# Kernel optimization log

Measured on AMD Instinct MI355X. Metric: run time of the kernel, lower is better.

The kernel has to match this reference:

```python
import jax, jax.numpy as jnp
import numpy as np

IN_FEATURES = 4096
OUT_FEATURES = 11008
BATCH, SEQ = 8, 16


def setup_inputs() -> dict:
    key = jax.random.key(0)
    k_in, k_w, k_s, k_b = jax.random.split(key, 4)
    inp = jax.random.normal(k_in, (BATCH, SEQ, IN_FEATURES), dtype=jnp.float32)
    # int8 weights in [-128, 127], as torch.randint(-128, 127, ...)
    quantized_weights = jax.random.randint(
        k_w, (OUT_FEATURES, IN_FEATURES), -128, 127, dtype=jnp.int32
    ).astype(jnp.int8)
    scales = jax.random.normal(k_s, (OUT_FEATURES,), dtype=jnp.float32)
    bias = jax.random.normal(k_b, (1, OUT_FEATURES), dtype=jnp.float32)
    return {"input": inp, "quantized_weights": quantized_weights,
            "scales": scales, "bias": bias}


def reference(input, quantized_weights, scales, bias):
    # dequantize weight to activation dtype, then linear: y = x @ W^T
    w = quantized_weights.astype(input.dtype)  # [O, I]
    out = jnp.einsum("bsi,oi->bso", input, w)  # [B, S, O]
    out = out * scales  # per-output-channel scale
    out = out + bias    # bias shape [1, O] broadcasts
    return out
```

## Files before the change

### kernel.cpp

```cpp
#include <hip/hip_runtime.h>
#include <stdint.h>


#define M_ROWS 128
#define K_DIM  4096
#define N_DIM  11008
#define CHUNKS 64
#define NT128  (N_DIM / 128)
#define KSPLIT 8
#define CPB    (CHUNKS / KSPLIT)
#define XP_BYTES (M_ROWS * K_DIM * 2)
#define PART_U32 ((size_t)64 * N_DIM)

typedef __attribute__((ext_vector_type(8))) short bf16x8;
typedef __attribute__((ext_vector_type(4))) float f32x4;
typedef const unsigned __attribute__((address_space(1)))* gas1_t;
typedef unsigned __attribute__((address_space(3)))* las3_t;

__device__ __forceinline__ unsigned bf16_rn(float f) {
  unsigned u = __float_as_uint(f);
  return (u + 0x7FFFu + ((u >> 16) & 1u)) >> 16;
}
__device__ __forceinline__ unsigned pk2(int a, int b) {
  unsigned lo = __float_as_uint((float)a), hi = __float_as_uint((float)b);
#if __has_builtin(__builtin_amdgcn_perm)
  return __builtin_amdgcn_perm(hi, lo, 0x07060302u);
#else
  return (hi & 0xFFFF0000u) | (lo >> 16);
#endif
}

__device__ __forceinline__ void gload_lds16(const void* g, void* lds) {
#if __has_builtin(__builtin_amdgcn_global_load_lds)
  __builtin_amdgcn_global_load_lds((gas1_t)g, (las3_t)(size_t)(unsigned)(size_t)lds,
                                   16, 0, 0);
#else
  *(uint4*)lds = *(const uint4*)g;
#endif
}

#define BAR()    asm volatile("s_barrier" ::: "memory")
#define WBAR12() asm volatile("s_waitcnt vmcnt(12)\n\ts_barrier" ::: "memory")
#define WBAR6()  asm volatile("s_waitcnt vmcnt(6)\n\ts_barrier" ::: "memory")
#define WBAR0()  asm volatile("s_waitcnt vmcnt(0)\n\ts_barrier" ::: "memory")

__global__ __launch_bounds__(256) void pack_x_kernel(
    const float* __restrict__ x, unsigned short* __restrict__ xp) {
  int tid  = blockIdx.x * 256 + threadIdx.x;
  int lane = tid & 63;
  int h    = (tid >> 6) & 1;
  int mf   = (tid >> 7) & 7;
  int kk   = tid >> 10;
  int m     = mf * 16 + (lane & 15);
  int kbase = kk * 64 + h * 32 + ((lane >> 4) * 8);
  const float* src = x + (size_t)m * K_DIM + kbase;
  float4 f0 = *(const float4*)(src);
  float4 f1 = *(const float4*)(src + 4);
  float v[8] = {f0.x, f0.y, f0.z, f0.w, f1.x, f1.y, f1.z, f1.w};
  unsigned po[4];
#pragma unroll
  for (int i = 0; i < 4; ++i)
    po[i] = bf16_rn(v[2 * i]) | (bf16_rn(v[2 * i + 1]) << 16);
  *(uint4*)(xp + (size_t)tid * 8) = *(uint4*)po;
}

struct BReg { uint4 v[4]; };

__global__ __launch_bounds__(512, 4) void gemm8w_kernel(
    const unsigned short* __restrict__ xp,
    const int* __restrict__ wq,
    unsigned* __restrict__ part) {
  __shared__ char As[3 * 16384];

  const int tid  = threadIdx.x;
  const int lane = tid & 63;
  const int w    = tid >> 6;
  const int nt   = blockIdx.x;
  const int kz   = blockIdx.y;
  const int kk0  = kz * CPB;
  const size_t n0 = (size_t)nt * 128 + (size_t)w * 16;
  const int l15 = lane & 15, lh = lane >> 4;

  const char* agp = (const char*)xp + (size_t)kk0 * 16384 + tid * 16;
  const int* bptr = wq + (n0 + (size_t)l15) * K_DIM + (size_t)kk0 * 64 + lh * 8;

  f32x4 acc[8];
  {
    f32x4 z = {0.f, 0.f, 0.f, 0.f};
#pragma unroll
    for (int i = 0; i < 8; ++i) acc[i] = z;
  }

  auto STAGE = [&](int t, int bufOff) {
    gload_lds16(agp + (size_t)t * 16384,        As + bufOff + tid * 16);
    gload_lds16(agp + (size_t)t * 16384 + 8192, As + bufOff + tid * 16 + 8192);
  };
  auto LOADB = [&](int t, BReg& R) {
    const int* bp = bptr + t * 64;
    R.v[0] = *(const uint4*)(bp);
    R.v[1] = *(const uint4*)(bp + 4);
    R.v[2] = *(const uint4*)(bp + 32);
    R.v[3] = *(const uint4*)(bp + 36);
  };
  auto COMP = [&](const char* ab, BReg& R) {
    bf16x8 cv[2];
#pragma unroll
    for (int s = 0; s < 2; ++s) {
      union { unsigned u[4]; bf16x8 b; } c;
      c.u[0] = pk2((int)R.v[s * 2].x,     (int)R.v[s * 2].y);
      c.u[1] = pk2((int)R.v[s * 2].z,     (int)R.v[s * 2].w);
      c.u[2] = pk2((int)R.v[s * 2 + 1].x, (int)R.v[s * 2 + 1].y);
      c.u[3] = pk2((int)R.v[s * 2 + 1].z, (int)R.v[s * 2 + 1].w);
      cv[s] = c.b;
    }
#pragma unroll
    for (int mf = 0; mf < 8; ++mf)
#pragma unroll
      for (int s = 0; s < 2; ++s) {
        bf16x8 a = *(const bf16x8*)(ab + (mf * 2 + s) * 1024 + lane * 16);
        acc[mf] = __builtin_amdgcn_mfma_f32_16x16x32_bf16(a, cv[s], acc[mf], 0, 0, 0);
      }
  };

#define PHASE(T, CBUF, NBUF, RC, RN)              \
    LOADB((T) + 2, RN);                           \
    BAR();                                        \
    STAGE((T) + 2, (NBUF) * 16384);               \
    WBAR12();                                     \
    COMP(As + (CBUF) * 16384, RC);

  BReg R0, R1, R2;
  STAGE(0, 0);
  LOADB(0, R0);
  STAGE(1, 16384);
  LOADB(1, R1);

#pragma unroll 1
  for (int t = 0; t < 6; t += 3) {
    PHASE(t + 0, 0, 2, R0, R2);
    PHASE(t + 1, 1, 0, R1, R0);
    PHASE(t + 2, 2, 1, R2, R1);
  }
  WBAR6();
  COMP(As + 0 * 16384, R0);
  WBAR0();
  COMP(As + 1 * 16384, R1);
#undef PHASE

  unsigned* pb = part + (size_t)kz * PART_U32 + n0 + l15;
#pragma unroll
  for (int mf = 0; mf < 8; ++mf) {
    const int mb = mf * 16 + lh * 4;
    unsigned u0 = bf16_rn(acc[mf][0]) | (bf16_rn(acc[mf][1]) << 16);
    unsigned u1 = bf16_rn(acc[mf][2]) | (bf16_rn(acc[mf][3]) << 16);
    pb[(size_t)(mb >> 1) * N_DIM]       = u0;
    pb[(size_t)((mb >> 1) + 1) * N_DIM] = u1;
  }
}

__global__ __launch_bounds__(256) void reduce_kernel(
    const unsigned* __restrict__ part, const float* __restrict__ scales,
    const float* __restrict__ bias, float* __restrict__ out) {
  const int mp = blockIdx.y;
  const int c4 = blockIdx.x * 256 + threadIdx.x;
  if (c4 >= N_DIM / 4) return;
  const size_t n = (size_t)c4 * 4;
  float s0[4] = {0.f, 0.f, 0.f, 0.f};
  float s1[4] = {0.f, 0.f, 0.f, 0.f};
#pragma unroll
  for (int z = 0; z < KSPLIT; ++z) {
    uint4 q = *(const uint4*)(part + (size_t)z * PART_U32 + (size_t)mp * N_DIM + n);
    const unsigned uu[4] = {q.x, q.y, q.z, q.w};
#pragma unroll
    for (int j = 0; j < 4; ++j) {
      s0[j] += __uint_as_float(uu[j] << 16);
      s1[j] += __uint_as_float(uu[j] & 0xFFFF0000u);
    }
  }
  float4 sc = *(const float4*)(scales + n);
  float4 bi = *(const float4*)(bias + n);
  const float scv[4] = {sc.x, sc.y, sc.z, sc.w};
  const float biv[4] = {bi.x, bi.y, bi.z, bi.w};
  float4 r0, r1;
  float* o0 = out + (size_t)(2 * mp) * N_DIM + n;
  float* o1 = out + (size_t)(2 * mp + 1) * N_DIM + n;
  r0.x = scv[0] * s0[0] + biv[0];  r1.x = scv[0] * s1[0] + biv[0];
  r0.y = scv[1] * s0[1] + biv[1];  r1.y = scv[1] * s1[1] + biv[1];
  r0.z = scv[2] * s0[2] + biv[2];  r1.z = scv[2] * s1[2] + biv[2];
  r0.w = scv[3] * s0[3] + biv[3];  r1.w = scv[3] * s1[3] + biv[3];
  *(float4*)o0 = r0;
  *(float4*)o1 = r1;
}

__global__ __launch_bounds__(256) void naive_kernel(
    const float* __restrict__ x, const int* __restrict__ wq,
    const float* __restrict__ scales, const float* __restrict__ bias,
    float* __restrict__ out) {
  const int n = blockIdx.x * 256 + threadIdx.x;
  const int m = blockIdx.y;
  const float* xr = x + (size_t)m * K_DIM;
  const int* wr = wq + (size_t)n * K_DIM;
  float s = 0.f;
  for (int k = 0; k < K_DIM; k += 4) {
    float4 xv = *(const float4*)(xr + k);
    int4  wv = *(const int4*)(wr + k);
    s += xv.x * (float)wv.x + xv.y * (float)wv.y +
         xv.z * (float)wv.z + xv.w * (float)wv.w;
  }
  out[(size_t)m * N_DIM + n] = scales[n] * s + bias[n];
}

extern "C" void kernel_launch(void* const* d_in, const int* in_sizes, int n_in,
                              void* d_out, int out_size, void* d_ws, size_t ws_size,
                              hipStream_t stream) {
  const float* x      = (const float*)d_in[0];
  const int* wq       = (const int*)d_in[1];
  const float* scales = (const float*)d_in[2];
  const float* bias   = (const float*)d_in[3];
  float* out          = (float*)d_out;

  const size_t need = (size_t)XP_BYTES + (size_t)KSPLIT * PART_U32 * 4;
  if (ws_size < need) {
    naive_kernel<<<dim3(N_DIM / 256, M_ROWS), 256, 0, stream>>>(x, wq, scales, bias, out);
    return;
  }
  unsigned short* xp = (unsigned short*)d_ws;
  unsigned* part     = (unsigned*)((char*)d_ws + XP_BYTES);

  pack_x_kernel<<<256, 256, 0, stream>>>(x, xp);
  gemm8w_kernel<<<dim3(NT128, KSPLIT), 512, 0, stream>>>(xp, wq, part);
  reduce_kernel<<<dim3((N_DIM / 4 + 255) / 256, 64), 256, 0, stream>>>(
      part, scales, bias, out);
}
```

Baseline: 51.54 us.

## Convert GEMM to persistent blocks pulling work items from an atomic counter

The GEMM launch changes from one block per (N-tile, K-split) pair, 86x8 = 688 blocks, to 512 persistent blocks. Each block takes work items dynamically through a global atomic counter, which the pack kernel resets to zero. The aim is to spread the tail of the 688 items more evenly and reduce launch and wave-quantization imbalance. In exchange it adds an atomic and two block barriers per item, and items are ordered N-tile first so concurrent blocks share K-slices of x.

```diff
diff --git a/kernel.cpp b/kernel.cpp
--- a/kernel.cpp
+++ b/kernel.cpp
@@ -9,7 +9,11 @@
 #define NT128  (N_DIM / 128)
 #define KSPLIT 8
 #define CPB    (CHUNKS / KSPLIT)
+#define NITEMS (NT128 * KSPLIT)
+#define GBLOCKS 512
 #define XP_BYTES (M_ROWS * K_DIM * 2)
+#define CTR_OFF  XP_BYTES
+#define PART_OFF (XP_BYTES + 256)
 #define PART_U32 ((size_t)64 * N_DIM)
 
 typedef __attribute__((ext_vector_type(8))) short bf16x8;
@@ -45,7 +49,9 @@
 #define WBAR0()  asm volatile("s_waitcnt vmcnt(0)\n\ts_barrier" ::: "memory")
 
 __global__ __launch_bounds__(256) void pack_x_kernel(
-    const float* __restrict__ x, unsigned short* __restrict__ xp) {
+    const float* __restrict__ x, unsigned short* __restrict__ xp,
+    int* __restrict__ counter) {
+  if (blockIdx.x == 0 && threadIdx.x == 0) *counter = 0;
   int tid  = blockIdx.x * 256 + threadIdx.x;
   int lane = tid & 63;
   int h    = (tid >> 6) & 1;
@@ -69,58 +75,68 @@
 __global__ __launch_bounds__(512, 4) void gemm8w_kernel(
     const unsigned short* __restrict__ xp,
     const int* __restrict__ wq,
-    unsigned* __restrict__ part) {
+    unsigned* __restrict__ part,
+    int* __restrict__ counter) {
   __shared__ char As[3 * 16384];
+  __shared__ int itemLds;
 
   const int tid  = threadIdx.x;
   const int lane = tid & 63;
   const int w    = tid >> 6;
-  const int nt   = blockIdx.x;
-  const int kz   = blockIdx.y;
-  const int kk0  = kz * CPB;
-  const size_t n0 = (size_t)nt * 128 + (size_t)w * 16;
   const int l15 = lane & 15, lh = lane >> 4;
 
-  const char* agp = (const char*)xp + (size_t)kk0 * 16384 + tid * 16;
-  const int* bptr = wq + (n0 + (size_t)l15) * K_DIM + (size_t)kk0 * 64 + lh * 8;
-
-  f32x4 acc[8];
-  {
-    f32x4 z = {0.f, 0.f, 0.f, 0.f};
-#pragma unroll
-    for (int i = 0; i < 8; ++i) acc[i] = z;
-  }
-
-  auto STAGE = [&](int t, int bufOff) {
-    gload_lds16(agp + (size_t)t * 16384,        As + bufOff + tid * 16);
-    gload_lds16(agp + (size_t)t * 16384 + 8192, As + bufOff + tid * 16 + 8192);
-  };
-  auto LOADB = [&](int t, BReg& R) {
-    const int* bp = bptr + t * 64;
-    R.v[0] = *(const uint4*)(bp);
-    R.v[1] = *(const uint4*)(bp + 4);
-    R.v[2] = *(const uint4*)(bp + 32);
-    R.v[3] = *(const uint4*)(bp + 36);
-  };
-  auto COMP = [&](const char* ab, BReg& R) {
-    bf16x8 cv[2];
-#pragma unroll
-    for (int s = 0; s < 2; ++s) {
-      union { unsigned u[4]; bf16x8 b; } c;
-      c.u[0] = pk2((int)R.v[s * 2].x,     (int)R.v[s * 2].y);
-      c.u[1] = pk2((int)R.v[s * 2].z,     (int)R.v[s * 2].w);
-      c.u[2] = pk2((int)R.v[s * 2 + 1].x, (int)R.v[s * 2 + 1].y);
-      c.u[3] = pk2((int)R.v[s * 2 + 1].z, (int)R.v[s * 2 + 1].w);
-      cv[s] = c.b;
-    }
-#pragma unroll
-    for (int mf = 0; mf < 8; ++mf)
+  for (;;) {
+    if (tid == 0) itemLds = atomicAdd(counter, 1);
+    __syncthreads();
+    const int item = itemLds;
+    __syncthreads();
+    if (item >= NITEMS) return;
+
+    const int nt = item % NT128;
+    const int kz = item / NT128;
+    const int kk0 = kz * CPB;
+    const size_t n0 = (size_t)nt * 128 + (size_t)w * 16;
+
+    const char* agp = (const char*)xp + (size_t)kk0 * 16384 + tid * 16;
+    const int* bptr = wq + (n0 + (size_t)l15) * K_DIM + (size_t)kk0 * 64 + lh * 8;
+
+    f32x4 acc[8];
+    {
+      f32x4 z = {0.f, 0.f, 0.f, 0.f};
+#pragma unroll
+      for (int i = 0; i < 8; ++i) acc[i] = z;
+    }
+
+    auto STAGE = [&](int t, int bufOff) {
+      gload_lds16(agp + (size_t)t * 16384,        As + bufOff + tid * 16);
+      gload_lds16(agp + (size_t)t * 16384 + 8192, As + bufOff + tid * 16 + 8192);
+    };
+    auto LOADB = [&](int t, BReg& R) {
+      const int* bp = bptr + t * 64;
+      R.v[0] = *(const uint4*)(bp);
+      R.v[1] = *(const uint4*)(bp + 4);
+      R.v[2] = *(const uint4*)(bp + 32);
+      R.v[3] = *(const uint4*)(bp + 36);
+    };
+    auto COMP = [&](const char* ab, BReg& R) {
+      bf16x8 cv[2];
 #pragma unroll
       for (int s = 0; s < 2; ++s) {
-        bf16x8 a = *(const bf16x8*)(ab + (mf * 2 + s) * 1024 + lane * 16);
-        acc[mf] = __builtin_amdgcn_mfma_f32_16x16x32_bf16(a, cv[s], acc[mf], 0, 0, 0);
+        union { unsigned u[4]; bf16x8 b; } c;
+        c.u[0] = pk2((int)R.v[s * 2].x,     (int)R.v[s * 2].y);
+        c.u[1] = pk2((int)R.v[s * 2].z,     (int)R.v[s * 2].w);
+        c.u[2] = pk2((int)R.v[s * 2 + 1].x, (int)R.v[s * 2 + 1].y);
+        c.u[3] = pk2((int)R.v[s * 2 + 1].z, (int)R.v[s * 2 + 1].w);
+        cv[s] = c.b;
       }
-  };
+#pragma unroll
+      for (int mf = 0; mf < 8; ++mf)
+#pragma unroll
+        for (int s = 0; s < 2; ++s) {
+          bf16x8 a = *(const bf16x8*)(ab + (mf * 2 + s) * 1024 + lane * 16);
+          acc[mf] = __builtin_amdgcn_mfma_f32_16x16x32_bf16(a, cv[s], acc[mf], 0, 0, 0);
+        }
+    };
 
 #define PHASE(T, CBUF, NBUF, RC, RN)              \
     LOADB((T) + 2, RN);                           \
@@ -129,32 +145,33 @@
     WBAR12();                                     \
     COMP(As + (CBUF) * 16384, RC);
 
-  BReg R0, R1, R2;
-  STAGE(0, 0);
-  LOADB(0, R0);
-  STAGE(1, 16384);
-  LOADB(1, R1);
+    BReg R0, R1, R2;
+    STAGE(0, 0);
+    LOADB(0, R0);
+    STAGE(1, 16384);
+    LOADB(1, R1);
 
 #pragma unroll 1
-  for (int t = 0; t < 6; t += 3) {
-    PHASE(t + 0, 0, 2, R0, R2);
-    PHASE(t + 1, 1, 0, R1, R0);
-    PHASE(t + 2, 2, 1, R2, R1);
-  }
-  WBAR6();
-  COMP(As + 0 * 16384, R0);
-  WBAR0();
-  COMP(As + 1 * 16384, R1);
+    for (int t = 0; t < 6; t += 3) {
+      PHASE(t + 0, 0, 2, R0, R2);
+      PHASE(t + 1, 1, 0, R1, R0);
+      PHASE(t + 2, 2, 1, R2, R1);
+    }
+    WBAR6();
+    COMP(As + 0 * 16384, R0);
+    WBAR0();
+    COMP(As + 1 * 16384, R1);
 #undef PHASE
 
-  unsigned* pb = part + (size_t)kz * PART_U32 + n0 + l15;
-#pragma unroll
-  for (int mf = 0; mf < 8; ++mf) {
-    const int mb = mf * 16 + lh * 4;
-    unsigned u0 = bf16_rn(acc[mf][0]) | (bf16_rn(acc[mf][1]) << 16);
-    unsigned u1 = bf16_rn(acc[mf][2]) | (bf16_rn(acc[mf][3]) << 16);
-    pb[(size_t)(mb >> 1) * N_DIM]       = u0;
-    pb[(size_t)((mb >> 1) + 1) * N_DIM] = u1;
+    unsigned* pb = part + (size_t)kz * PART_U32 + n0 + l15;
+#pragma unroll
+    for (int mf = 0; mf < 8; ++mf) {
+      const int mb = mf * 16 + lh * 4;
+      unsigned u0 = bf16_rn(acc[mf][0]) | (bf16_rn(acc[mf][1]) << 16);
+      unsigned u1 = bf16_rn(acc[mf][2]) | (bf16_rn(acc[mf][3]) << 16);
+      pb[(size_t)(mb >> 1) * N_DIM]       = u0;
+      pb[(size_t)((mb >> 1) + 1) * N_DIM] = u1;
+    }
   }
 }
 
@@ -219,16 +236,17 @@
   const float* bias   = (const float*)d_in[3];
   float* out          = (float*)d_out;
 
-  const size_t need = (size_t)XP_BYTES + (size_t)KSPLIT * PART_U32 * 4;
+  const size_t need = (size_t)PART_OFF + (size_t)KSPLIT * PART_U32 * 4;
   if (ws_size < need) {
     naive_kernel<<<dim3(N_DIM / 256, M_ROWS), 256, 0, stream>>>(x, wq, scales, bias, out);
     return;
   }
   unsigned short* xp = (unsigned short*)d_ws;
-  unsigned* part     = (unsigned*)((char*)d_ws + XP_BYTES);
-
-  pack_x_kernel<<<256, 256, 0, stream>>>(x, xp);
-  gemm8w_kernel<<<dim3(NT128, KSPLIT), 512, 0, stream>>>(xp, wq, part);
+  int* counter       = (int*)((char*)d_ws + CTR_OFF);
+  unsigned* part     = (unsigned*)((char*)d_ws + PART_OFF);
+
+  pack_x_kernel<<<256, 256, 0, stream>>>(x, xp, counter);
+  gemm8w_kernel<<<dim3(GBLOCKS), 512, 0, stream>>>(xp, wq, part, counter);
   reduce_kernel<<<dim3((N_DIM / 4 + 255) / 256, 64), 256, 0, stream>>>(
       part, scales, bias, out);
 }
```

New measurement: 55.35 us. +7.4%, slower.
